# Optimization experiments

Measured on AMD Instinct MI355X. Metric: run time of the kernel, lower is better.

## Reference

```python
import jax, jax.numpy as jnp
import numpy as np

D = 4096

def setup_inputs() -> dict:
    key = jax.random.key(0)
    k1, k2 = jax.random.split(key)
    matrix = jax.random.normal(k1, (D, D), dtype=jnp.float32)
    n = jax.random.normal(k2, (D,), dtype=jnp.float32)
    return {"matrix": matrix, "n": n}

def reference(matrix, n):
    # matrix @ matrix.T is PSD; adding a strictly positive softplus diagonal makes it SPD
    m = matrix @ matrix.T + jnp.diag(jax.nn.softplus(n))
    return jnp.linalg.cholesky(m)
```

## Files before the change

### kernel.cpp

```cpp
#include <hip/hip_runtime.h>
#include <math.h>

#define D 4096
#define NB 128
#define KC 32
#define NT (D / NB)
#define LDP 40

typedef __attribute__((ext_vector_type(8))) short short8;
typedef __attribute__((ext_vector_type(4))) float f32x4;
typedef __attribute__((ext_vector_type(4))) unsigned int uint4v;
typedef unsigned short ush;

__device__ __forceinline__ float softplusf(float x) {
  return fmaxf(x, 0.0f) + log1pf(expf(-fabsf(x)));
}

struct HL { unsigned int h, l; };

__device__ __forceinline__ HL split2(float x0, float x1) {
  unsigned int b0 = __float_as_uint(x0), b1 = __float_as_uint(x1);
  unsigned int h0 = b0 & 0xFFFF0000u, h1 = b1 & 0xFFFF0000u;
  float r0 = x0 - __uint_as_float(h0);
  float r1 = x1 - __uint_as_float(h1);
  HL out;
  out.h = h1 | (h0 >> 16);
  out.l = (__float_as_uint(r1) & 0xFFFF0000u) | (__float_as_uint(r0) >> 16);
  return out;
}

__device__ __forceinline__ void split1(float x, ush& h, ush& l) {
  unsigned int b = __float_as_uint(x);
  unsigned int hb = b & 0xFFFF0000u;
  float r = x - __uint_as_float(hb);
  h = (ush)(hb >> 16);
  l = (ush)(__float_as_uint(r) >> 16);
}

__device__ void potrf_factor(float (*Ls)[NB + 1]) {
  int tid = threadIdx.x;
  int lane = tid & 63, wid = tid >> 6;
  int tx = tid & 15, ty = tid >> 4;

  for (int pp = 0; pp < 8; ++pp) {
    int pc0 = pp * 16;
    if (wid == 0) {
      int ra = lane, rb = lane + 64;
      bool va = (ra >= pc0), vb = (rb >= pc0);
      float xa[16], xb[16];
#pragma unroll
      for (int c = 0; c < 16; ++c) {
        xa[c] = va ? Ls[ra][pc0 + c] : 0.0f;
        xb[c] = vb ? Ls[rb][pc0 + c] : 0.0f;
      }
#pragma unroll
      for (int j = 0; j < 16; ++j) {
        int jj = pc0 + j;
        float dv = (jj < 64) ? __shfl(xa[j], jj) : __shfl(xb[j], jj - 64);
        float di = __builtin_amdgcn_rcpf(dv);
        float ta = (ra > jj) ? xa[j] * di : 0.0f;
        float tb = (rb > jj) ? xb[j] * di : 0.0f;
#pragma unroll
        for (int c = j + 1; c < 16; ++c) {
          int rc = pc0 + c;
          float lc = (rc < 64) ? __shfl(xa[j], rc) : __shfl(xb[j], rc - 64);
          xa[c] -= ta * lc;
          xb[c] -= tb * lc;
        }
      }
#pragma unroll
      for (int c = 0; c < 16; ++c) {
        int rc = pc0 + c;
        float dc = (rc < 64) ? __shfl(xa[c], rc) : __shfl(xb[c], rc - 64);
        float sc = __builtin_amdgcn_rsqf(dc);
        xa[c] *= sc;
        xb[c] *= sc;
      }
      if (va) {
#pragma unroll
        for (int c = 0; c < 16; ++c) Ls[ra][pc0 + c] = xa[c];
      }
      if (vb) {
#pragma unroll
        for (int c = 0; c < 16; ++c) Ls[rb][pc0 + c] = xb[c];
      }
    }
    __syncthreads();

    int s0 = pc0 + 16;
    if (s0 < NB) {
      int r0 = ty * 8, c0 = tx * 8;
      if (r0 >= s0 && c0 >= s0) {
        float acc[8][8];
#pragma unroll
        for (int rr = 0; rr < 8; ++rr) {
          float4 m0 = *(const float4*)&Ls[r0 + rr][c0];
          float4 m1 = *(const float4*)&Ls[r0 + rr][c0 + 4];
          acc[rr][0] = m0.x; acc[rr][1] = m0.y; acc[rr][2] = m0.z; acc[rr][3] = m0.w;
          acc[rr][4] = m1.x; acc[rr][5] = m1.y; acc[rr][6] = m1.z; acc[rr][7] = m1.w;
        }
#pragma unroll
        for (int q = 0; q < 16; ++q) {
          float av[8], bv[8];
#pragma unroll
          for (int rr = 0; rr < 8; ++rr) av[rr] = Ls[r0 + rr][pc0 + q];
#pragma unroll
          for (int cc = 0; cc < 8; ++cc) bv[cc] = Ls[c0 + cc][pc0 + q];
#pragma unroll
          for (int rr = 0; rr < 8; ++rr)
#pragma unroll
            for (int cc = 0; cc < 8; ++cc) acc[rr][cc] -= av[rr] * bv[cc];
        }
#pragma unroll
        for (int rr = 0; rr < 8; ++rr) {
          *(float4*)&Ls[r0 + rr][c0] =
              make_float4(acc[rr][0], acc[rr][1], acc[rr][2], acc[rr][3]);
          *(float4*)&Ls[r0 + rr][c0 + 4] =
              make_float4(acc[rr][4], acc[rr][5], acc[rr][6], acc[rr][7]);
        }
      }
    }
    __syncthreads();
  }
}

__device__ void potrf_store(float* Msrc, float (*Ls)[NB + 1]) {
  int tid = threadIdx.x;
  for (int idx = tid; idx < NB * NB; idx += 256) {
    int i = idx >> 7, j = idx & (NB - 1);
    Msrc[(size_t)i * D + j] = (j <= i) ? Ls[i][j] : 0.0f;
  }
}

__global__ __launch_bounds__(256) void potrf_kernel(float* __restrict__ M, int kb)
{
  __shared__ float Ls[NB][NB + 1];
  int tid = threadIdx.x;
  float* Msrc = M + (size_t)kb * D + kb;
  for (int idx = tid; idx < NB * NB; idx += 256) {
    int i = idx >> 7, j = idx & (NB - 1);
    Ls[i][j] = Msrc[(size_t)i * D + j];
  }
  __syncthreads();
  potrf_factor(Ls);
  potrf_store(Msrc, Ls);
}

__global__ __launch_bounds__(256) void convA_kernel(
    const float* __restrict__ A, ush* __restrict__ AhG, ush* __restrict__ AlG)
{
  size_t idx = ((size_t)blockIdx.x * 256 + threadIdx.x) * 8;
  float4 v0 = *(const float4*)(A + idx);
  float4 v1 = *(const float4*)(A + idx + 4);
  HL p0 = split2(v0.x, v0.y), p1 = split2(v0.z, v0.w);
  HL p2 = split2(v1.x, v1.y), p3 = split2(v1.z, v1.w);
  uint4v h = {p0.h, p1.h, p2.h, p3.h};
  uint4v l = {p0.l, p1.l, p2.l, p3.l};
  *(uint4v*)(AhG + idx) = h;
  *(uint4v*)(AlG + idx) = l;
}

template <bool SHA>
__global__ __launch_bounds__(256) void syrk0_kernel(
    const float* __restrict__ Asrc, const float* __restrict__ nvec,
    float* __restrict__ Mout,
    const ush* __restrict__ AhG, const ush* __restrict__ AlG)
{
  __shared__ ush Ah[NB][LDP], Al[NB][LDP];
  __shared__ ush Bh[NB][LDP], Bl[NB][LDP];

  int b = blockIdx.x;
  int ti = (int)((sqrtf(8.0f * (float)b + 1.0f) - 1.0f) * 0.5f);
  while ((ti + 1) * (ti + 2) / 2 <= b) ++ti;
  while (ti * (ti + 1) / 2 > b) --ti;
  int tj = b - ti * (ti + 1) / 2;
  int row0 = ti * NB, col0 = tj * NB;

  int tid = threadIdx.x;
  int lane = tid & 63, wid = tid >> 6;
  int wr = wid >> 1, wc = wid & 1;
  int srow = tid >> 1;
  int scg = (tid & 1) * 16;

  f32x4 acc[4][4];
#pragma unroll
  for (int m = 0; m < 4; ++m)
#pragma unroll
    for (int n = 0; n < 4; ++n) acc[m][n] = (f32x4){0.f, 0.f, 0.f, 0.f};

  int lr16 = lane & 15, kof = (lane >> 4) * 8;

  for (int kk = 0; kk < D; kk += KC) {
    if (SHA) {
      const ush* pah = AhG + (size_t)(row0 + srow) * D + kk + scg;
      const ush* pal = AlG + (size_t)(row0 + srow) * D + kk + scg;
      const ush* pbh = AhG + (size_t)(col0 + srow) * D + kk + scg;
      const ush* pbl = AlG + (size_t)(col0 + srow) * D + kk + scg;
      short8 ah0 = *(const short8*)pah, ah1 = *(const short8*)(pah + 8);
      short8 al0 = *(const short8*)pal, al1 = *(const short8*)(pal + 8);
      short8 bh0 = *(const short8*)pbh, bh1 = *(const short8*)(pbh + 8);
      short8 bl0 = *(const short8*)pbl, bl1 = *(const short8*)(pbl + 8);
      __syncthreads();
      *(short8*)&Ah[srow][scg] = ah0;  *(short8*)&Ah[srow][scg + 8] = ah1;
      *(short8*)&Al[srow][scg] = al0;  *(short8*)&Al[srow][scg + 8] = al1;
      *(short8*)&Bh[srow][scg] = bh0;  *(short8*)&Bh[srow][scg + 8] = bh1;
      *(short8*)&Bl[srow][scg] = bl0;  *(short8*)&Bl[srow][scg + 8] = bl1;
    } else {
      const float* pa = Asrc + (size_t)(row0 + srow) * D + kk + scg;
      const float* pb = Asrc + (size_t)(col0 + srow) * D + kk + scg;
      float4 av0 = *(const float4*)(pa + 0), av1 = *(const float4*)(pa + 4);
      float4 av2 = *(const float4*)(pa + 8), av3 = *(const float4*)(pa + 12);
      float4 bv0 = *(const float4*)(pb + 0), bv1 = *(const float4*)(pb + 4);
      float4 bv2 = *(const float4*)(pb + 8), bv3 = *(const float4*)(pb + 12);
      __syncthreads();
      {
        HL p0 = split2(av0.x, av0.y), p1 = split2(av0.z, av0.w);
        HL p2 = split2(av1.x, av1.y), p3 = split2(av1.z, av1.w);
        HL p4 = split2(av2.x, av2.y), p5 = split2(av2.z, av2.w);
        HL p6 = split2(av3.x, av3.y), p7 = split2(av3.z, av3.w);
        uint4v h0 = {p0.h, p1.h, p2.h, p3.h}, l0 = {p0.l, p1.l, p2.l, p3.l};
        uint4v h1 = {p4.h, p5.h, p6.h, p7.h}, l1 = {p4.l, p5.l, p6.l, p7.l};
        *(uint4v*)&Ah[srow][scg] = h0;  *(uint4v*)&Ah[srow][scg + 8] = h1;
        *(uint4v*)&Al[srow][scg] = l0;  *(uint4v*)&Al[srow][scg + 8] = l1;
      }
      {
        HL p0 = split2(bv0.x, bv0.y), p1 = split2(bv0.z, bv0.w);
        HL p2 = split2(bv1.x, bv1.y), p3 = split2(bv1.z, bv1.w);
        HL p4 = split2(bv2.x, bv2.y), p5 = split2(bv2.z, bv2.w);
        HL p6 = split2(bv3.x, bv3.y), p7 = split2(bv3.z, bv3.w);
        uint4v h0 = {p0.h, p1.h, p2.h, p3.h}, l0 = {p0.l, p1.l, p2.l, p3.l};
        uint4v h1 = {p4.h, p5.h, p6.h, p7.h}, l1 = {p4.l, p5.l, p6.l, p7.l};
        *(uint4v*)&Bh[srow][scg] = h0;  *(uint4v*)&Bh[srow][scg + 8] = h1;
        *(uint4v*)&Bl[srow][scg] = l0;  *(uint4v*)&Bl[srow][scg + 8] = l1;
      }
    }
    __syncthreads();

    short8 ah[4], al[4], bh[4], bl[4];
#pragma unroll
    for (int m = 0; m < 4; ++m) {
      int r = wr * 64 + m * 16 + lr16;
      ah[m] = *(const short8*)&Ah[r][kof];
      al[m] = *(const short8*)&Al[r][kof];
    }
#pragma unroll
    for (int n = 0; n < 4; ++n) {
      int c = wc * 64 + n * 16 + lr16;
      bh[n] = *(const short8*)&Bh[c][kof];
      bl[n] = *(const short8*)&Bl[c][kof];
    }
#pragma unroll
    for (int m = 0; m < 4; ++m)
#pragma unroll
      for (int n = 0; n < 4; ++n) {
        acc[m][n] = __builtin_amdgcn_mfma_f32_16x16x32_bf16(ah[m], bh[n], acc[m][n], 0, 0, 0);
        acc[m][n] = __builtin_amdgcn_mfma_f32_16x16x32_bf16(ah[m], bl[n], acc[m][n], 0, 0, 0);
        acc[m][n] = __builtin_amdgcn_mfma_f32_16x16x32_bf16(al[m], bh[n], acc[m][n], 0, 0, 0);
      }
  }

  int cl = lane & 15, rg = (lane >> 4) * 4;
#pragma unroll
  for (int m = 0; m < 4; ++m) {
#pragma unroll
    for (int n = 0; n < 4; ++n) {
      int gi0 = row0 + wr * 64 + m * 16 + rg;
      int gj = col0 + wc * 64 + n * 16 + cl;
#pragma unroll
      for (int r = 0; r < 4; ++r) {
        int gi = gi0 + r;
        float v = acc[m][n][r];
        if (gi == gj) v += softplusf(nvec[gi]);
        Mout[(size_t)gi * D + gj] = v;
      }
    }
  }

  if (ti > tj) {
    float4 z = make_float4(0.f, 0.f, 0.f, 0.f);
    int zr = tid >> 1;
    int zc0 = (tid & 1) * 64;
    float* zp = Mout + (size_t)(col0 + zr) * D + row0 + zc0;
#pragma unroll
    for (int q = 0; q < 16; ++q) *(float4*)(zp + 4 * q) = z;
  }
}

template <bool SH>
__global__ __launch_bounds__(256) void trsm_kernel(
    float* __restrict__ M, int kb, ush* __restrict__ shH, ush* __restrict__ shL)
{
  __shared__ float Ls[NB][NB + 1];
  __shared__ float dinv[NB];
  int tid = threadIdx.x;
  const float* Lsrc = M + (size_t)kb * D + kb;
  for (int idx = tid; idx < NB * NB; idx += 256) {
    int i = idx >> 7, j = idx & (NB - 1);
    Ls[i][j] = Lsrc[(size_t)i * D + j];
  }
  __syncthreads();
  if (tid < NB) dinv[tid] = 1.0f / Ls[tid][tid];
  __syncthreads();
  int lane = tid & 63, w = tid >> 6;
  size_t r0 = (size_t)(kb + NB) + (size_t)blockIdx.x * 8 + w * 2;
  float* p0 = M + r0 * D + kb;
  float* p1 = p0 + D;
  float x0l = p0[lane], x0h = p0[64 + lane];
  float x1l = p1[lane], x1h = p1[64 + lane];
  for (int p = 0; p < 64; ++p) {
    float dv = dinv[p];
    float xp0 = __shfl(x0l, p) * dv;
    float xp1 = __shfl(x1l, p) * dv;
    float Llo = Ls[lane][p];
    float Lhi = Ls[64 + lane][p];
    if (lane == p)      { x0l = xp0; x1l = xp1; }
    else if (lane > p)  { x0l -= xp0 * Llo; x1l -= xp1 * Llo; }
    x0h -= xp0 * Lhi;
    x1h -= xp1 * Lhi;
  }
  for (int p = 64; p < NB; ++p) {
    int q = p - 64;
    float dv = dinv[p];
    float xp0 = __shfl(x0h, q) * dv;
    float xp1 = __shfl(x1h, q) * dv;
    float Lhi = Ls[64 + lane][p];
    if (lane == q)      { x0h = xp0; x1h = xp1; }
    else if (lane > q)  { x0h -= xp0 * Lhi; x1h -= xp1 * Lhi; }
  }
  p0[lane] = x0l; p0[64 + lane] = x0h;
  p1[lane] = x1l; p1[64 + lane] = x1h;
  if (SH) {
    ush h, l;
    split1(x0l, h, l);
    shH[r0 * NB + lane] = h;        shL[r0 * NB + lane] = l;
    split1(x0h, h, l);
    shH[r0 * NB + 64 + lane] = h;   shL[r0 * NB + 64 + lane] = l;
    split1(x1l, h, l);
    shH[(r0 + 1) * NB + lane] = h;      shL[(r0 + 1) * NB + lane] = l;
    split1(x1h, h, l);
    shH[(r0 + 1) * NB + 64 + lane] = h; shL[(r0 + 1) * NB + 64 + lane] = l;
  }
}

__device__ void gemm_bt(const float* __restrict__ Ap, const float* __restrict__ Bp,
                        f32x4 (&acc)[4][4],
                        ush (*Ah)[LDP], ush (*Al)[LDP],
                        ush (*Bh)[LDP], ush (*Bl)[LDP])
{
  int tid = threadIdx.x;
  int lane = tid & 63, wid = tid >> 6;
  int wr = wid >> 1, wc = wid & 1;
  int srow = tid >> 1, scg = (tid & 1) * 16;
  int lr16 = lane & 15, kof = (lane >> 4) * 8;

  for (int kk = 0; kk < NB; kk += KC) {
    const float* pa = Ap + (size_t)srow * D + kk + scg;
    const float* pb = Bp + (size_t)srow * D + kk + scg;
    float4 av0 = *(const float4*)(pa + 0), av1 = *(const float4*)(pa + 4);
    float4 av2 = *(const float4*)(pa + 8), av3 = *(const float4*)(pa + 12);
    float4 bv0 = *(const float4*)(pb + 0), bv1 = *(const float4*)(pb + 4);
    float4 bv2 = *(const float4*)(pb + 8), bv3 = *(const float4*)(pb + 12);

    __syncthreads();
    {
      HL p0 = split2(av0.x, av0.y), p1 = split2(av0.z, av0.w);
      HL p2 = split2(av1.x, av1.y), p3 = split2(av1.z, av1.w);
      HL p4 = split2(av2.x, av2.y), p5 = split2(av2.z, av2.w);
      HL p6 = split2(av3.x, av3.y), p7 = split2(av3.z, av3.w);
      uint4v h0 = {p0.h, p1.h, p2.h, p3.h}, l0 = {p0.l, p1.l, p2.l, p3.l};
      uint4v h1 = {p4.h, p5.h, p6.h, p7.h}, l1 = {p4.l, p5.l, p6.l, p7.l};
      *(uint4v*)&Ah[srow][scg] = h0;  *(uint4v*)&Ah[srow][scg + 8] = h1;
      *(uint4v*)&Al[srow][scg] = l0;  *(uint4v*)&Al[srow][scg + 8] = l1;
    }
    {
      HL p0 = split2(bv0.x, bv0.y), p1 = split2(bv0.z, bv0.w);
      HL p2 = split2(bv1.x, bv1.y), p3 = split2(bv1.z, bv1.w);
      HL p4 = split2(bv2.x, bv2.y), p5 = split2(bv2.z, bv2.w);
      HL p6 = split2(bv3.x, bv3.y), p7 = split2(bv3.z, bv3.w);
      uint4v h0 = {p0.h, p1.h, p2.h, p3.h}, l0 = {p0.l, p1.l, p2.l, p3.l};
      uint4v h1 = {p4.h, p5.h, p6.h, p7.h}, l1 = {p4.l, p5.l, p6.l, p7.l};
      *(uint4v*)&Bh[srow][scg] = h0;  *(uint4v*)&Bh[srow][scg + 8] = h1;
      *(uint4v*)&Bl[srow][scg] = l0;  *(uint4v*)&Bl[srow][scg + 8] = l1;
    }
    __syncthreads();

    short8 ah[4], al[4], bh[4], bl[4];
#pragma unroll
    for (int m = 0; m < 4; ++m) {
      int r = wr * 64 + m * 16 + lr16;
      ah[m] = *(const short8*)&Ah[r][kof];
      al[m] = *(const short8*)&Al[r][kof];
    }
#pragma unroll
    for (int n = 0; n < 4; ++n) {
      int c = wc * 64 + n * 16 + lr16;
      bh[n] = *(const short8*)&Bh[c][kof];
      bl[n] = *(const short8*)&Bl[c][kof];
    }
#pragma unroll
    for (int m = 0; m < 4; ++m)
#pragma unroll
      for (int n = 0; n < 4; ++n) {
        acc[m][n] = __builtin_amdgcn_mfma_f32_16x16x32_bf16(ah[m], bh[n], acc[m][n], 0, 0, 0);
        acc[m][n] = __builtin_amdgcn_mfma_f32_16x16x32_bf16(ah[m], bl[n], acc[m][n], 0, 0, 0);
        acc[m][n] = __builtin_amdgcn_mfma_f32_16x16x32_bf16(al[m], bh[n], acc[m][n], 0, 0, 0);
      }
  }
}

__device__ void gemm_bt_sh(const ush* __restrict__ AhG, const ush* __restrict__ AlG,
                           const ush* __restrict__ BhG, const ush* __restrict__ BlG,
                           f32x4 (&acc)[4][4],
                           ush (*Ah)[LDP], ush (*Al)[LDP],
                           ush (*Bh)[LDP], ush (*Bl)[LDP])
{
  int tid = threadIdx.x;
  int lane = tid & 63, wid = tid >> 6;
  int wr = wid >> 1, wc = wid & 1;
  int srow = tid >> 1, scg = (tid & 1) * 16;
  int lr16 = lane & 15, kof = (lane >> 4) * 8;

  for (int kk = 0; kk < NB; kk += KC) {
    const ush* pah = AhG + (size_t)srow * NB + kk + scg;
    const ush* pal = AlG + (size_t)srow * NB + kk + scg;
    const ush* pbh = BhG + (size_t)srow * NB + kk + scg;
    const ush* pbl = BlG + (size_t)srow * NB + kk + scg;
    short8 vah0 = *(const short8*)(pah), vah1 = *(const short8*)(pah + 8);
    short8 val0 = *(const short8*)(pal), val1 = *(const short8*)(pal + 8);
    short8 vbh0 = *(const short8*)(pbh), vbh1 = *(const short8*)(pbh + 8);
    short8 vbl0 = *(const short8*)(pbl), vbl1 = *(const short8*)(pbl + 8);

    __syncthreads();
    *(short8*)&Ah[srow][scg] = vah0;  *(short8*)&Ah[srow][scg + 8] = vah1;
    *(short8*)&Al[srow][scg] = val0;  *(short8*)&Al[srow][scg + 8] = val1;
    *(short8*)&Bh[srow][scg] = vbh0;  *(short8*)&Bh[srow][scg + 8] = vbh1;
    *(short8*)&Bl[srow][scg] = vbl0;  *(short8*)&Bl[srow][scg + 8] = vbl1;
    __syncthreads();

    short8 ah[4], al[4], bh[4], bl[4];
#pragma unroll
    for (int m = 0; m < 4; ++m) {
      int r = wr * 64 + m * 16 + lr16;
      ah[m] = *(const short8*)&Ah[r][kof];
      al[m] = *(const short8*)&Al[r][kof];
    }
#pragma unroll
    for (int n = 0; n < 4; ++n) {
      int c = wc * 64 + n * 16 + lr16;
      bh[n] = *(const short8*)&Bh[c][kof];
      bl[n] = *(const short8*)&Bl[c][kof];
    }
#pragma unroll
    for (int m = 0; m < 4; ++m)
#pragma unroll
      for (int n = 0; n < 4; ++n) {
        acc[m][n] = __builtin_amdgcn_mfma_f32_16x16x32_bf16(ah[m], bh[n], acc[m][n], 0, 0, 0);
        acc[m][n] = __builtin_amdgcn_mfma_f32_16x16x32_bf16(ah[m], bl[n], acc[m][n], 0, 0, 0);
        acc[m][n] = __builtin_amdgcn_mfma_f32_16x16x32_bf16(al[m], bh[n], acc[m][n], 0, 0, 0);
      }
  }
}

template <bool SH>
__global__ __launch_bounds__(256) void syrk1_kernel(
    float* __restrict__ M, int kb,
    const ush* __restrict__ shH, const ush* __restrict__ shL)
{
  __shared__ __align__(16) unsigned char smem[66560];
  ush (*Ah)[LDP] = (ush(*)[LDP])(smem);
  ush (*Al)[LDP] = (ush(*)[LDP])(smem + 10240);
  ush (*Bh)[LDP] = (ush(*)[LDP])(smem + 20480);
  ush (*Bl)[LDP] = (ush(*)[LDP])(smem + 30720);
  float (*Ls)[NB + 1] = (float(*)[NB + 1])smem;

  float* Mout = M + (size_t)(kb + NB) * D + (kb + NB);
  const float* Xsrc = M + (size_t)(kb + NB) * D + kb;

  int s = blockIdx.x;
  int ti = (int)((sqrtf(8.0f * (float)s + 1.0f) - 1.0f) * 0.5f);
  while ((ti + 1) * (ti + 2) / 2 <= s) ++ti;
  while (ti * (ti + 1) / 2 > s) --ti;
  int tj = s - ti * (ti + 1) / 2;
  int row0 = ti * NB, col0 = tj * NB;

  int tid = threadIdx.x;
  int lane = tid & 63, wid = tid >> 6;
  int wr = wid >> 1, wc = wid & 1;
  int cl = lane & 15, rg = (lane >> 4) * 4;

  f32x4 acc[4][4];
#pragma unroll
  for (int m = 0; m < 4; ++m)
#pragma unroll
    for (int n = 0; n < 4; ++n) acc[m][n] = (f32x4){0.f, 0.f, 0.f, 0.f};

  if (SH) {
    size_t ra = (size_t)(kb + NB + row0) * NB;
    size_t rb = (size_t)(kb + NB + col0) * NB;
    gemm_bt_sh(shH + ra, shL + ra, shH + rb, shL + rb, acc, Ah, Al, Bh, Bl);
  } else {
    gemm_bt(Xsrc + (size_t)row0 * D, Xsrc + (size_t)col0 * D, acc, Ah, Al, Bh, Bl);
  }

  if (s == 0) {
    __syncthreads();
#pragma unroll
    for (int m = 0; m < 4; ++m)
#pragma unroll
      for (int n = 0; n < 4; ++n) {
        int li0 = wr * 64 + m * 16 + rg;
        int lj = wc * 64 + n * 16 + cl;
#pragma unroll
        for (int r = 0; r < 4; ++r) {
          int li = li0 + r;
          Ls[li][lj] = Mout[(size_t)li * D + lj] - acc[m][n][r];
        }
      }
    __syncthreads();
    potrf_factor(Ls);
    potrf_store(Mout, Ls);
    return;
  }

#pragma unroll
  for (int m = 0; m < 4; ++m) {
#pragma unroll
    for (int n = 0; n < 4; ++n) {
      int gi0 = row0 + wr * 64 + m * 16 + rg;
      int gj = col0 + wc * 64 + n * 16 + cl;
#pragma unroll
      for (int r = 0; r < 4; ++r) {
        int gi = gi0 + r;
        Mout[(size_t)gi * D + gj] -= acc[m][n][r];
      }
    }
  }
}

extern "C" void kernel_launch(void* const* d_in, const int* in_sizes, int n_in,
                              void* d_out, int out_size, void* d_ws, size_t ws_size,
                              hipStream_t stream)
{
  (void)in_sizes; (void)n_in; (void)out_size;
  const float* A  = (const float*)d_in[0];
  const float* nv = (const float*)d_in[1];
  float* M = (float*)d_out;

  const size_t xsh_elems = (size_t)D * NB;
  const size_t ash_elems = (size_t)D * D;
  const size_t need_x = 2 * xsh_elems * sizeof(ush);
  const size_t need_a = need_x + 2 * ash_elems * sizeof(ush);
  bool shX = (ws_size >= need_x);
  bool shA = (ws_size >= need_a);
  ush* xH = (ush*)d_ws;
  ush* xL = xH + xsh_elems;
  ush* aH = xL + xsh_elems;
  ush* aL = aH + ash_elems;

  if (shA) {
    convA_kernel<<<(int)(ash_elems / 8 / 256), 256, 0, stream>>>(A, aH, aL);
    syrk0_kernel<true><<<NT * (NT + 1) / 2, 256, 0, stream>>>(A, nv, M, aH, aL);
  } else {
    syrk0_kernel<false><<<NT * (NT + 1) / 2, 256, 0, stream>>>(A, nv, M, nullptr, nullptr);
  }
  potrf_kernel<<<1, 256, 0, stream>>>(M, 0);

  for (int k = 0; k <= 30; ++k) {
    int kb = k * NB;
    int T = D - kb - NB;
    int t = T / NB;
    if (shX) {
      trsm_kernel<true><<<T / 8, 256, 0, stream>>>(M, kb, xH, xL);
      syrk1_kernel<true><<<t * (t + 1) / 2, 256, 0, stream>>>(M, kb, xH, xL);
    } else {
      trsm_kernel<false><<<T / 8, 256, 0, stream>>>(M, kb, nullptr, nullptr);
      syrk1_kernel<false><<<t * (t + 1) / 2, 256, 0, stream>>>(M, kb, nullptr, nullptr);
    }
  }
}
```

Measured before the change: 3.707 ms.

## Apply trailing SYRK updates two panels at a time with double-buffered split panels

The blocked Cholesky loop now processes two 128-wide panels per iteration. After the first panel's TRSM, a narrow kernel updates only the next panel column and factors its diagonal block. Once the second TRSM has run, one trailing SYRK applies both panels' contributions, with K=256, from even/odd workspace banks. This halves the number of full trailing-matrix read-modify-write passes and SYRK launches, at the cost of extra launches and twice the workspace.

```diff
diff --git a/kernel.cpp b/kernel.cpp
--- a/kernel.cpp
+++ b/kernel.cpp
@@ -461,9 +461,8 @@
   }
 }
 
-template <bool SH>
-__global__ __launch_bounds__(256) void syrk1_kernel(
-    float* __restrict__ M, int kb,
+__global__ __launch_bounds__(256) void syrk_col_kernel(
+    float* __restrict__ M, int k0,
     const ush* __restrict__ shH, const ush* __restrict__ shL)
 {
   __shared__ __align__(16) unsigned char smem[66560];
@@ -473,6 +472,129 @@
   ush (*Bl)[LDP] = (ush(*)[LDP])(smem + 30720);
   float (*Ls)[NB + 1] = (float(*)[NB + 1])smem;
 
+  int jcol = k0 + 1;
+  int i = jcol + blockIdx.x;
+
+  int tid = threadIdx.x;
+  int lane = tid & 63, wid = tid >> 6;
+  int wr = wid >> 1, wc = wid & 1;
+  int cl = lane & 15, rg = (lane >> 4) * 4;
+
+  f32x4 acc[4][4];
+#pragma unroll
+  for (int m = 0; m < 4; ++m)
+#pragma unroll
+    for (int n = 0; n < 4; ++n) acc[m][n] = (f32x4){0.f, 0.f, 0.f, 0.f};
+
+  size_t ra = (size_t)(i * NB) * NB;
+  size_t rb = (size_t)(jcol * NB) * NB;
+  gemm_bt_sh(shH + ra, shL + ra, shH + rb, shL + rb, acc, Ah, Al, Bh, Bl);
+
+  float* Mt = M + (size_t)(i * NB) * D + jcol * NB;
+  if (blockIdx.x == 0) {
+    __syncthreads();
+#pragma unroll
+    for (int m = 0; m < 4; ++m)
+#pragma unroll
+      for (int n = 0; n < 4; ++n) {
+        int li0 = wr * 64 + m * 16 + rg;
+        int lj = wc * 64 + n * 16 + cl;
+#pragma unroll
+        for (int r = 0; r < 4; ++r)
+          Ls[li0 + r][lj] = Mt[(size_t)(li0 + r) * D + lj] - acc[m][n][r];
+      }
+    __syncthreads();
+    potrf_factor(Ls);
+    potrf_store(Mt, Ls);
+    return;
+  }
+#pragma unroll
+  for (int m = 0; m < 4; ++m)
+#pragma unroll
+    for (int n = 0; n < 4; ++n) {
+      int li0 = wr * 64 + m * 16 + rg;
+      int lj = wc * 64 + n * 16 + cl;
+#pragma unroll
+      for (int r = 0; r < 4; ++r)
+        Mt[(size_t)(li0 + r) * D + lj] -= acc[m][n][r];
+    }
+}
+
+__global__ __launch_bounds__(256) void syrk256_kernel(
+    float* __restrict__ M, int k0,
+    const ush* __restrict__ shHE, const ush* __restrict__ shLE,
+    const ush* __restrict__ shHO, const ush* __restrict__ shLO)
+{
+  __shared__ __align__(16) unsigned char smem[66560];
+  ush (*Ah)[LDP] = (ush(*)[LDP])(smem);
+  ush (*Al)[LDP] = (ush(*)[LDP])(smem + 10240);
+  ush (*Bh)[LDP] = (ush(*)[LDP])(smem + 20480);
+  ush (*Bl)[LDP] = (ush(*)[LDP])(smem + 30720);
+  float (*Ls)[NB + 1] = (float(*)[NB + 1])smem;
+
+  int base = k0 + 2;
+  int s = blockIdx.x;
+  int tp = (int)((sqrtf(8.0f * (float)s + 1.0f) - 1.0f) * 0.5f);
+  while ((tp + 1) * (tp + 2) / 2 <= s) ++tp;
+  while (tp * (tp + 1) / 2 > s) --tp;
+  int tq = s - tp * (tp + 1) / 2;
+  int i = base + tp, j = base + tq;
+
+  int tid = threadIdx.x;
+  int lane = tid & 63, wid = tid >> 6;
+  int wr = wid >> 1, wc = wid & 1;
+  int cl = lane & 15, rg = (lane >> 4) * 4;
+
+  f32x4 acc[4][4];
+#pragma unroll
+  for (int m = 0; m < 4; ++m)
+#pragma unroll
+    for (int n = 0; n < 4; ++n) acc[m][n] = (f32x4){0.f, 0.f, 0.f, 0.f};
+
+  size_t ra = (size_t)(i * NB) * NB;
+  size_t rb = (size_t)(j * NB) * NB;
+  gemm_bt_sh(shHE + ra, shLE + ra, shHE + rb, shLE + rb, acc, Ah, Al, Bh, Bl);
+  gemm_bt_sh(shHO + ra, shLO + ra, shHO + rb, shLO + rb, acc, Ah, Al, Bh, Bl);
+
+  float* Mt = M + (size_t)(i * NB) * D + j * NB;
+  if (s == 0) {
+    __syncthreads();
+#pragma unroll
+    for (int m = 0; m < 4; ++m)
+#pragma unroll
+      for (int n = 0; n < 4; ++n) {
+        int li0 = wr * 64 + m * 16 + rg;
+        int lj = wc * 64 + n * 16 + cl;
+#pragma unroll
+        for (int r = 0; r < 4; ++r)
+          Ls[li0 + r][lj] = Mt[(size_t)(li0 + r) * D + lj] - acc[m][n][r];
+      }
+    __syncthreads();
+    potrf_factor(Ls);
+    potrf_store(Mt, Ls);
+    return;
+  }
+#pragma unroll
+  for (int m = 0; m < 4; ++m)
+#pragma unroll
+    for (int n = 0; n < 4; ++n) {
+      int li0 = wr * 64 + m * 16 + rg;
+      int lj = wc * 64 + n * 16 + cl;
+#pragma unroll
+      for (int r = 0; r < 4; ++r)
+        Mt[(size_t)(li0 + r) * D + lj] -= acc[m][n][r];
+    }
+}
+
+__global__ __launch_bounds__(256) void syrk1_fb_kernel(float* __restrict__ M, int kb)
+{
+  __shared__ __align__(16) unsigned char smem[66560];
+  ush (*Ah)[LDP] = (ush(*)[LDP])(smem);
+  ush (*Al)[LDP] = (ush(*)[LDP])(smem + 10240);
+  ush (*Bh)[LDP] = (ush(*)[LDP])(smem + 20480);
+  ush (*Bl)[LDP] = (ush(*)[LDP])(smem + 30720);
+  float (*Ls)[NB + 1] = (float(*)[NB + 1])smem;
+
   float* Mout = M + (size_t)(kb + NB) * D + (kb + NB);
   const float* Xsrc = M + (size_t)(kb + NB) * D + kb;
 
@@ -494,13 +616,7 @@
 #pragma unroll
     for (int n = 0; n < 4; ++n) acc[m][n] = (f32x4){0.f, 0.f, 0.f, 0.f};
 
-  if (SH) {
-    size_t ra = (size_t)(kb + NB + row0) * NB;
-    size_t rb = (size_t)(kb + NB + col0) * NB;
-    gemm_bt_sh(shH + ra, shL + ra, shH + rb, shL + rb, acc, Ah, Al, Bh, Bl);
-  } else {
-    gemm_bt(Xsrc + (size_t)row0 * D, Xsrc + (size_t)col0 * D, acc, Ah, Al, Bh, Bl);
-  }
+  gemm_bt(Xsrc + (size_t)row0 * D, Xsrc + (size_t)col0 * D, acc, Ah, Al, Bh, Bl);
 
   if (s == 0) {
     __syncthreads();
@@ -511,30 +627,24 @@
         int li0 = wr * 64 + m * 16 + rg;
         int lj = wc * 64 + n * 16 + cl;
 #pragma unroll
-        for (int r = 0; r < 4; ++r) {
-          int li = li0 + r;
-          Ls[li][lj] = Mout[(size_t)li * D + lj] - acc[m][n][r];
-        }
+        for (int r = 0; r < 4; ++r)
+          Ls[li0 + r][lj] = Mout[(size_t)(li0 + r) * D + lj] - acc[m][n][r];
       }
     __syncthreads();
     potrf_factor(Ls);
     potrf_store(Mout, Ls);
     return;
   }
-
-#pragma unroll
-  for (int m = 0; m < 4; ++m) {
+#pragma unroll
+  for (int m = 0; m < 4; ++m)
 #pragma unroll
     for (int n = 0; n < 4; ++n) {
       int gi0 = row0 + wr * 64 + m * 16 + rg;
       int gj = col0 + wc * 64 + n * 16 + cl;
 #pragma unroll
-      for (int r = 0; r < 4; ++r) {
-        int gi = gi0 + r;
-        Mout[(size_t)gi * D + gj] -= acc[m][n][r];
-      }
-    }
-  }
+      for (int r = 0; r < 4; ++r)
+        Mout[(size_t)(gi0 + r) * D + gj] -= acc[m][n][r];
+    }
 }
 
 extern "C" void kernel_launch(void* const* d_in, const int* in_sizes, int n_in,
@@ -546,16 +656,18 @@
   const float* nv = (const float*)d_in[1];
   float* M = (float*)d_out;
 
-  const size_t xsh_elems = (size_t)D * NB;
+  const size_t bank = (size_t)D * NB;
   const size_t ash_elems = (size_t)D * D;
-  const size_t need_x = 2 * xsh_elems * sizeof(ush);
+  const size_t need_x = 4 * bank * sizeof(ush);
   const size_t need_a = need_x + 2 * ash_elems * sizeof(ush);
   bool shX = (ws_size >= need_x);
   bool shA = (ws_size >= need_a);
-  ush* xH = (ush*)d_ws;
-  ush* xL = xH + xsh_elems;
-  ush* aH = xL + xsh_elems;
-  ush* aL = aH + ash_elems;
+  ush* xHE = (ush*)d_ws;
+  ush* xLE = xHE + bank;
+  ush* xHO = xLE + bank;
+  ush* xLO = xHO + bank;
+  ush* aH  = xLO + bank;
+  ush* aL  = aH + ash_elems;
 
   if (shA) {
     convA_kernel<<<(int)(ash_elems / 8 / 256), 256, 0, stream>>>(A, aH, aL);
@@ -565,16 +677,29 @@
   }
   potrf_kernel<<<1, 256, 0, stream>>>(M, 0);
 
-  for (int k = 0; k <= 30; ++k) {
-    int kb = k * NB;
-    int T = D - kb - NB;
-    int t = T / NB;
-    if (shX) {
-      trsm_kernel<true><<<T / 8, 256, 0, stream>>>(M, kb, xH, xL);
-      syrk1_kernel<true><<<t * (t + 1) / 2, 256, 0, stream>>>(M, kb, xH, xL);
-    } else {
+  if (shX) {
+    for (int p = 0; p < NT / 2; ++p) {
+      int k0 = 2 * p, kb0 = k0 * NB;
+      int T0 = D - kb0 - NB;
+      trsm_kernel<true><<<T0 / 8, 256, 0, stream>>>(M, kb0, xHE, xLE);
+      int t1 = NT - 1 - k0;
+      syrk_col_kernel<<<t1, 256, 0, stream>>>(M, k0, xHE, xLE);
+      int T1 = D - (k0 + 1) * NB - NB;
+      if (T1 > 0)
+        trsm_kernel<true><<<T1 / 8, 256, 0, stream>>>(M, (k0 + 1) * NB, xHO, xLO);
+      int t2 = NT - 2 - k0;
+      if (t2 > 0) {
+        int C2 = t2 * (t2 + 1) / 2;
+        syrk256_kernel<<<C2, 256, 0, stream>>>(M, k0, xHE, xLE, xHO, xLO);
+      }
+    }
+  } else {
+    for (int k = 0; k <= 30; ++k) {
+      int kb = k * NB;
+      int T = D - kb - NB;
+      int t = T / NB;
       trsm_kernel<false><<<T / 8, 256, 0, stream>>>(M, kb, nullptr, nullptr);
-      syrk1_kernel<false><<<t * (t + 1) / 2, 256, 0, stream>>>(M, kb, nullptr, nullptr);
-    }
-  }
-}
+      syrk1_fb_kernel<<<t * (t + 1) / 2, 256, 0, stream>>>(M, kb);
+    }
+  }
+}
```

New measurement: 3.755 ms. No clear change (+1.3%).
